# Kernel optimization log

Hardware: AMD Instinct MI355X
Metric: run time of the kernel (lower is better)

## Reference

```python
import jax, jax.numpy as jnp
import numpy as np

N_NODES = 50000
N_EDGES = 800000
N_GRAPHS = 64
IN_DIM = 128
HID = 256
N_LAYERS = 4
N_PROT = 5
N_CLASSES = 1
EPS = 1e-12


def setup_inputs() -> dict:
    key = jax.random.key(0)
    ks = jax.random.split(key, 10)
    h = jax.random.normal(ks[0], (N_NODES, IN_DIM), jnp.float32)
    src = jax.random.randint(ks[1], (N_EDGES,), 0, N_NODES, dtype=jnp.int32)
    dst = jax.random.randint(ks[2], (N_EDGES,), 0, N_NODES, dtype=jnp.int32)
    graph_id = jnp.sort(jax.random.randint(ks[3], (N_NODES,), 0, N_GRAPHS, dtype=jnp.int32))
    W_emb = jax.random.normal(ks[4], (IN_DIM, HID), jnp.float32) * 0.05
    b_emb = jnp.zeros((HID,), jnp.float32)
    Ws = jax.random.normal(ks[5], (N_LAYERS, 2 * HID, HID), jnp.float32) * 0.05
    bs = jnp.zeros((N_LAYERS, HID), jnp.float32)
    p_pos = jax.random.uniform(ks[6], (N_PROT, HID), jnp.float32)
    p_neg = jax.random.uniform(ks[7], (N_PROT, HID), jnp.float32)
    W_fc = jax.random.normal(ks[8], (N_CLASSES, 2 * N_PROT), jnp.float32) * 0.1
    return dict(h=h, src=src, dst=dst, graph_id=graph_id, W_emb=W_emb,
                b_emb=b_emb, Ws=Ws, bs=bs, p_pos=p_pos, p_neg=p_neg, W_fc=W_fc)


def _segment_mean(x, seg, num):
    # sum over segments, divide by count (empty segments -> 0, like DGL mean)
    s = jax.ops.segment_sum(x, seg, num_segments=num)
    cnt = jax.ops.segment_sum(jnp.ones((x.shape[0],), x.dtype), seg, num_segments=num)
    return s / jnp.maximum(cnt, 1.0)[:, None]


def _forward(h, src, dst, graph_id, W_emb, b_emb, Ws, bs, p_pos, p_neg, W_fc):
    x = h @ W_emb + b_emb  # [N, HID]
    for l in range(N_LAYERS):
        # mean aggregation of neighbor messages (copy_src -> mean at dst)
        c = _segment_mean(x[src], dst, N_NODES)  # [N, HID]
        bundle = jnp.concatenate([x, c], axis=1) @ Ws[l] + bs[l]  # [N, HID]
        # F.normalize(p=2, dim=1) then relu activation, then residual add
        norm = jnp.linalg.norm(bundle, axis=1, keepdims=True)
        bundle = bundle / jnp.maximum(norm, EPS)
        x = x + jax.nn.relu(bundle)
    hg = _segment_mean(x, graph_id, N_GRAPHS)  # dgl.mean_nodes -> [G, HID]

    def sims(P):
        d = jnp.sum((hg[:, None, :] - P[None, :, :]) ** 2, axis=-1)  # [G, P]
        return jnp.log((d + 1.0) / (d + EPS))

    ss = jnp.concatenate([sims(p_pos), sims(p_neg)], axis=1)  # [G, 2P]
    y = ss @ W_fc.T  # [G, n_classes]
    return jax.nn.sigmoid(y).squeeze()


def reference(h, src, dst, graph_id, W_emb, b_emb, Ws, bs, p_pos, p_neg, W_fc):
    return _forward(h, src, dst, graph_id, W_emb, b_emb, Ws, bs, p_pos, p_neg, W_fc)
```

## Files before the change

kernel.cpp:

```cpp
#include <hip/hip_runtime.h>
#include <math.h>

#define N_NODESC 50000
#define NPAD 50048
#define N_EDGESC 800000
#define N_GRAPHSC 64
#define IN_DIMC 128
#define HIDC 256
#define N_LAYERSC 4
#define EPSV 1e-12f

#define NBUCK 196
#define EPB 4096
#define NBLK1 196

typedef __attribute__((ext_vector_type(8))) short short8;
typedef __attribute__((ext_vector_type(4))) float floatx4;
typedef __attribute__((ext_vector_type(2))) float floatx2;

__device__ __forceinline__ unsigned short f2b(float f) {
    union { float f; unsigned u; } v; v.f = f;
    unsigned r = v.u + 0x7FFFu + ((v.u >> 16) & 1u);
    return (unsigned short)(r >> 16);
}
__device__ __forceinline__ float blo(unsigned u) { return __uint_as_float(u << 16); }
__device__ __forceinline__ float bhi(unsigned u) { return __uint_as_float(u & 0xFFFF0000u); }
__device__ __forceinline__ unsigned pkb(float a, float b) {
    return (unsigned)f2b(a) | ((unsigned)f2b(b) << 16);
}
__device__ __forceinline__ float b2f(unsigned short s) {
    return __uint_as_float((unsigned)s << 16);
}
__device__ __forceinline__ unsigned char f2q(float v) {
    return (unsigned char)(__builtin_amdgcn_cvt_pk_fp8_f32(v, v, 0, false) & 0xFF);
}
__device__ __forceinline__ float q2f(unsigned u) {
    floatx2 t = __builtin_amdgcn_cvt_pk_f32_fp8(u, false);
    return t.x;
}
__device__ __forceinline__ unsigned pk4q(float a, float b, float c, float d) {
    unsigned lo = (unsigned)__builtin_amdgcn_cvt_pk_fp8_f32(a, b, 0, false) & 0xFFFFu;
    unsigned hi = (unsigned)__builtin_amdgcn_cvt_pk_fp8_f32(c, d, 0, false) << 16;
    return lo | hi;
}
__device__ __forceinline__ void ldscp16(const void* g, void* l) {
    __builtin_amdgcn_global_load_lds(
        (const __attribute__((address_space(1))) unsigned int*)g,
        (__attribute__((address_space(3))) unsigned int*)l, 16, 0, 0);
}

__global__ __launch_bounds__(128) void k_gbounds(const int* __restrict__ gid,
        int* __restrict__ gstart) {
    int g = threadIdx.x;
    if (g > N_GRAPHSC) return;
    int lo = 0, hi = N_NODESC;
    while (lo < hi) {
        int mid = (lo + hi) >> 1;
        if (gid[mid] < g) lo = mid + 1; else hi = mid;
    }
    gstart[g] = lo;
}

__global__ __launch_bounds__(256) void k_bcount(const int* __restrict__ dst,
        int* __restrict__ gbcnt) {
    __shared__ int bc[256];
    int t = threadIdx.x;
    bc[t] = 0;
    __syncthreads();
    int e0 = blockIdx.x * EPB;
    for (int i = t; i < EPB; i += 256) {
        int e = e0 + i;
        if (e < N_EDGESC) atomicAdd(&bc[dst[e] >> 8], 1);
    }
    __syncthreads();
    if (t < NBUCK && bc[t] > 0) atomicAdd(&gbcnt[t], bc[t]);
}

__global__ __launch_bounds__(256) void k_bscan(const int* __restrict__ gbcnt,
        int* __restrict__ boffB, int* __restrict__ gcurB) {
    __shared__ int s[256];
    int t = threadIdx.x;
    int v = (t < NBUCK) ? gbcnt[t] : 0;
    s[t] = v;
    __syncthreads();
    for (int d = 1; d < 256; d <<= 1) {
        int u = (t >= d) ? s[t - d] : 0;
        __syncthreads();
        s[t] += u;
        __syncthreads();
    }
    if (t < NBUCK) {
        int excl = s[t] - v;
        boffB[t] = excl;
        gcurB[t] = excl;
    }
    if (t == 0) boffB[NBUCK] = N_EDGESC;
}

__global__ __launch_bounds__(256) void k_bscatter(const int* __restrict__ src,
        const int* __restrict__ dst, int* __restrict__ gcurB,
        unsigned* __restrict__ ebpack) {
    __shared__ int bc[256];
    __shared__ int cur[256];
    int t = threadIdx.x;
    bc[t] = 0;
    __syncthreads();
    int e0 = blockIdx.x * EPB;
    for (int i = t; i < EPB; i += 256) {
        int e = e0 + i;
        if (e < N_EDGESC) atomicAdd(&bc[dst[e] >> 8], 1);
    }
    __syncthreads();
    if (t < NBUCK)
        cur[t] = (bc[t] > 0) ? atomicAdd(&gcurB[t], bc[t]) : 0;
    __syncthreads();
    for (int i = t; i < EPB; i += 256) {
        int e = e0 + i;
        if (e < N_EDGESC) {
            int d = dst[e];
            int b = d >> 8;
            int pos = atomicAdd(&cur[b], 1);
            ebpack[pos] = (unsigned)src[e] | ((unsigned)(d & 255) << 16);
        }
    }
}

__global__ __launch_bounds__(256) void k_bbuild(const unsigned* __restrict__ ebpack,
        const int* __restrict__ boffB, int* __restrict__ offs,
        unsigned short* __restrict__ esrc) {
    __shared__ int deg[256];
    __shared__ int lofs[256];
    __shared__ unsigned short img[12288];
    int b = blockIdx.x;
    int t = threadIdx.x;
    int bbase = boffB[b];
    int cnt = boffB[b + 1] - bbase;
    deg[t] = 0;
    __syncthreads();
    for (int i = t; i < cnt; i += 256)
        atomicAdd(&deg[ebpack[bbase + i] >> 16], 1);
    __syncthreads();
    int v = deg[t];
    lofs[t] = v;
    __syncthreads();
    for (int d = 1; d < 256; d <<= 1) {
        int u = (t >= d) ? lofs[t - d] : 0;
        __syncthreads();
        lofs[t] += u;
        __syncthreads();
    }
    int excl = lofs[t] - v;
    int node = b * 256 + t;
    if (node < N_NODESC) offs[node] = bbase + excl;
    if (b == NBUCK - 1 && t == 0) offs[N_NODESC] = N_EDGESC;
    deg[t] = excl;
    __syncthreads();
    for (int i = t; i < cnt; i += 256) {
        unsigned p = ebpack[bbase + i];
        int pos = atomicAdd(&deg[p >> 16], 1);
        img[pos] = (unsigned short)(p & 0xFFFF);
    }
    __syncthreads();
    for (int i = t; i < cnt; i += 256)
        esrc[bbase + i] = img[i];
}

__global__ __launch_bounds__(256) void k_wconv(const float* __restrict__ Wemb,
        const float* __restrict__ Ws, unsigned short* __restrict__ wsw,
        unsigned char* __restrict__ wq) {
    int idx = blockIdx.x * 256 + threadIdx.x;
    const int EMB = IN_DIMC * HIDC;
    const int LYR = 2 * HIDC * HIDC;
    if (idx >= EMB + N_LAYERSC * LYR) return;
    if (idx < EMB) {
        int k = idx >> 8, n = idx & 255;
        int off = (((k >> 5) * 16 + (n >> 4)) * 64 + ((((k >> 3) & 3) << 4) | (n & 15))) * 8 + (k & 7);
        wsw[off] = f2b(Wemb[idx]);
    } else {
        int r = idx - EMB;
        int l = r >> 17;
        int r2 = r & (LYR - 1);
        int k = r2 >> 8, n = r2 & 255;
        int off = (((k >> 5) * 16 + (n >> 4)) * 64 + ((((k >> 3) & 3) << 4) | (n & 15))) * 8 + (k & 7);
        wq[(size_t)l * LYR + off] = f2q(Ws[r]);
    }
}

__global__ __launch_bounds__(256) void k_aggregate(const unsigned char* __restrict__ xq,
        const int* __restrict__ offs, const unsigned short* __restrict__ esrc,
        unsigned char* __restrict__ cq) {
    int gidx = blockIdx.x * 256 + threadIdx.x;
    int node = gidx >> 5;
    int lane = threadIdx.x & 31;
    if (node >= N_NODESC) return;
    int beg = offs[node], end = offs[node + 1];
    float a[8];
    #pragma unroll
    for (int j = 0; j < 8; j++) a[j] = 0.f;
    size_t loff = (size_t)lane * 8;
    int e = beg;
    #define ACC8(v) do { \
        floatx2 t0 = __builtin_amdgcn_cvt_pk_f32_fp8((v).x, false); \
        floatx2 t1 = __builtin_amdgcn_cvt_pk_f32_fp8((v).x, true);  \
        floatx2 t2 = __builtin_amdgcn_cvt_pk_f32_fp8((v).y, false); \
        floatx2 t3 = __builtin_amdgcn_cvt_pk_f32_fp8((v).y, true);  \
        a[0] += t0.x; a[1] += t0.y; a[2] += t1.x; a[3] += t1.y;     \
        a[4] += t2.x; a[5] += t2.y; a[6] += t3.x; a[7] += t3.y;     \
    } while (0)
    for (; e + 8 <= end; e += 8) {
        int sidx[8];
        #pragma unroll
        for (int j = 0; j < 8; j++) sidx[j] = esrc[e + j];
        uint2 v[8];
        #pragma unroll
        for (int j = 0; j < 8; j++)
            v[j] = *(const uint2*)(xq + (size_t)sidx[j] * HIDC + loff);
        #pragma unroll
        for (int j = 0; j < 8; j++) ACC8(v[j]);
    }
    if (e + 4 <= end) {
        int sidx[4];
        #pragma unroll
        for (int j = 0; j < 4; j++) sidx[j] = esrc[e + j];
        uint2 v[4];
        #pragma unroll
        for (int j = 0; j < 4; j++)
            v[j] = *(const uint2*)(xq + (size_t)sidx[j] * HIDC + loff);
        #pragma unroll
        for (int j = 0; j < 4; j++) ACC8(v[j]);
        e += 4;
    }
    for (; e < end; e++) {
        uint2 v = *(const uint2*)(xq + (size_t)esrc[e] * HIDC + loff);
        ACC8(v);
    }
    #undef ACC8
    float w = 1.0f / (float)max(end - beg, 1);
    uint2 o;
    o.x = pk4q(a[0] * w, a[1] * w, a[2] * w, a[3] * w);
    o.y = pk4q(a[4] * w, a[5] * w, a[6] * w, a[7] * w);
    *(uint2*)(cq + (size_t)node * HIDC + loff) = o;
}

template<bool LAST>
__global__ __launch_bounds__(256, 6) void k_lgemm(unsigned short* __restrict__ xb,
        unsigned char* __restrict__ xq, const unsigned char* __restrict__ cq,
        const unsigned char* __restrict__ wq, const float* __restrict__ bias) {
    __shared__ unsigned long long panelA64[1024];
    __shared__ unsigned long long panelC64[1024];
    __shared__ float rs[32];
    unsigned char* panelA = (unsigned char*)panelA64;
    unsigned char* panelC = (unsigned char*)panelC64;
    int tid = threadIdx.x;
    int w = tid >> 6;
    int lane = tid & 63;
    int quad = lane >> 4;
    int l15 = lane & 15;
    int row0 = blockIdx.x * 32;

    {
        int sboff = w * 2048 + lane * 16;
        #pragma unroll
        for (int i = 0; i < 2; i++) {
            int ldsoff = sboff + i * 1024;
            int r = ldsoff >> 8;
            int ch = (ldsoff & 255) >> 4;
            int lc = ch ^ (r & 15);
            ldscp16(xq + (size_t)(row0 + r) * HIDC + lc * 16, &panelA[w * 2048 + i * 1024]);
            ldscp16(cq + (size_t)(row0 + r) * HIDC + lc * 16, &panelC[w * 2048 + i * 1024]);
        }
    }
    __syncthreads();

    floatx4 acc[2][4];
    #pragma unroll
    for (int mt = 0; mt < 2; mt++)
        #pragma unroll
        for (int n = 0; n < 4; n++)
            acc[mt][n] = (floatx4){0.f, 0.f, 0.f, 0.f};

    const unsigned char* bp = wq + ((size_t)(w * 4) * 64 + lane) * 8;

    #pragma unroll
    for (int st = 0; st < 16; st++) {
        const unsigned char* pan = (st < 8) ? panelA : panelC;
        int ks = st & 7;
        long long afr[2], bfr[4];
        #pragma unroll
        for (int mt = 0; mt < 2; mt++) {
            int row = mt * 16 + l15;
            int lc = ks * 2 + (quad >> 1);
            int phys = lc ^ (row & 15);
            afr[mt] = *(const long long*)&pan[row * 256 + phys * 16 + (quad & 1) * 8];
        }
        const unsigned char* wp = bp + (size_t)st * 8192;
        #pragma unroll
        for (int n = 0; n < 4; n++)
            bfr[n] = *(const long long*)(wp + n * 512);
        #pragma unroll
        for (int mt = 0; mt < 2; mt++)
            #pragma unroll
            for (int n = 0; n < 4; n++)
                acc[mt][n] = __builtin_amdgcn_mfma_f32_16x16x32_fp8_fp8(
                    afr[mt], bfr[n], acc[mt][n], 0, 0, 0);
    }

    float bv[4];
    #pragma unroll
    for (int n = 0; n < 4; n++) bv[n] = bias[w * 64 + n * 16 + l15];
    #pragma unroll
    for (int mt = 0; mt < 2; mt++)
        #pragma unroll
        for (int n = 0; n < 4; n++)
            #pragma unroll
            for (int r = 0; r < 4; r++)
                acc[mt][n][r] += bv[n];

    __syncthreads();
    if (tid < 32) rs[tid] = 0.f;
    __syncthreads();
    #pragma unroll
    for (int mt = 0; mt < 2; mt++) {
        #pragma unroll
        for (int r = 0; r < 4; r++) {
            float p = acc[mt][0][r] * acc[mt][0][r] + acc[mt][1][r] * acc[mt][1][r]
                    + acc[mt][2][r] * acc[mt][2][r] + acc[mt][3][r] * acc[mt][3][r];
            p += __shfl_xor(p, 1);
            p += __shfl_xor(p, 2);
            p += __shfl_xor(p, 4);
            p += __shfl_xor(p, 8);
            if (l15 == 0) atomicAdd(&rs[mt * 16 + quad * 4 + r], p);
        }
    }
    __syncthreads();

    #pragma unroll
    for (int mt = 0; mt < 2; mt++) {
        #pragma unroll
        for (int r = 0; r < 4; r++) {
            int lrow = mt * 16 + quad * 4 + r;
            int row = row0 + lrow;
            if (row < N_NODESC) {
                float inv = 1.0f / fmaxf(sqrtf(rs[mt * 16 + quad * 4 + r]), EPSV);
                #pragma unroll
                for (int n = 0; n < 4; n++) {
                    int col = w * 64 + n * 16 + l15;
                    int phys = (w * 4 + n) ^ (lrow & 15);
                    float xo = q2f((unsigned)panelA[lrow * 256 + phys * 16 + l15]);
                    float v = fmaxf(acc[mt][n][r] * inv, 0.f);
                    float nv = xo + v;
                    size_t idx = (size_t)row * HIDC + col;
                    if (LAST) xb[idx] = f2b(nv);
                    else      xq[idx] = f2q(nv);
                }
            }
        }
    }
}

__global__ __launch_bounds__(256, 4) void k_egemm(const float* __restrict__ h,
        const unsigned short* __restrict__ wsw, const float* __restrict__ bias,
        unsigned char* __restrict__ xq) {
    int tid = threadIdx.x;
    int wn = tid >> 6;
    int lane = tid & 63;
    int quad = lane >> 4;
    int l15 = lane & 15;
    int row0 = blockIdx.x * 32;

    floatx4 acc[2][4];
    #pragma unroll
    for (int mt = 0; mt < 2; mt++)
        #pragma unroll
        for (int n = 0; n < 4; n++)
            acc[mt][n] = (floatx4){0.f, 0.f, 0.f, 0.f};

    int r0 = row0 + l15;
    int r1 = row0 + 16 + l15;
    bool ok0 = r0 < N_NODESC, ok1 = r1 < N_NODESC;
    const float* h0 = h + (size_t)r0 * IN_DIMC + quad * 8;
    const float* h1 = h + (size_t)r1 * IN_DIMC + quad * 8;
    const unsigned short* bp = wsw + ((size_t)(wn * 4) * 64 + lane) * 8;

    #pragma unroll
    for (int ks = 0; ks < 4; ks++) {
        float4 f00 = ok0 ? *(const float4*)(h0 + ks * 32)     : (float4){0,0,0,0};
        float4 f01 = ok0 ? *(const float4*)(h0 + ks * 32 + 4) : (float4){0,0,0,0};
        float4 f10 = ok1 ? *(const float4*)(h1 + ks * 32)     : (float4){0,0,0,0};
        float4 f11 = ok1 ? *(const float4*)(h1 + ks * 32 + 4) : (float4){0,0,0,0};
        short8 afr[2], bfr[4];
        uint4 av;
        av.x = pkb(f00.x, f00.y); av.y = pkb(f00.z, f00.w);
        av.z = pkb(f01.x, f01.y); av.w = pkb(f01.z, f01.w);
        afr[0] = *(short8*)&av;
        av.x = pkb(f10.x, f10.y); av.y = pkb(f10.z, f10.w);
        av.z = pkb(f11.x, f11.y); av.w = pkb(f11.z, f11.w);
        afr[1] = *(short8*)&av;
        const unsigned short* wp = bp + (size_t)ks * 8192;
        #pragma unroll
        for (int n = 0; n < 4; n++)
            bfr[n] = *(const short8*)(wp + n * 512);
        #pragma unroll
        for (int mt = 0; mt < 2; mt++)
            #pragma unroll
            for (int n = 0; n < 4; n++)
                acc[mt][n] = __builtin_amdgcn_mfma_f32_16x16x32_bf16(
                    afr[mt], bfr[n], acc[mt][n], 0, 0, 0);
    }

    float bv[4];
    #pragma unroll
    for (int n = 0; n < 4; n++) bv[n] = bias[wn * 64 + n * 16 + l15];
    #pragma unroll
    for (int mt = 0; mt < 2; mt++) {
        #pragma unroll
        for (int r = 0; r < 4; r++) {
            int row = row0 + mt * 16 + quad * 4 + r;
            if (row < N_NODESC) {
                #pragma unroll
                for (int n = 0; n < 4; n++) {
                    int col = wn * 64 + n * 16 + l15;
                    float v = acc[mt][n][r] + bv[n];
                    xq[(size_t)row * HIDC + col] = f2q(v);
                }
            }
        }
    }
}

__global__ __launch_bounds__(256) void k_pool(const unsigned short* __restrict__ xb,
        const int* __restrict__ gstart, float* __restrict__ hg) {
    __shared__ float red[256][8];
    int g = blockIdx.x >> 2;
    int cq = blockIdx.x & 3;
    int t = threadIdx.x;
    int cchunk = t & 7;
    int rgrp = t >> 3;
    int col0 = cq * 64 + cchunk * 8;
    int beg = gstart[g], end = gstart[g + 1];
    float a[8];
    #pragma unroll
    for (int j = 0; j < 8; j++) a[j] = 0.f;
    for (int r = beg + rgrp; r < end; r += 32) {
        uint4 v = *(const uint4*)(xb + (size_t)r * HIDC + col0);
        a[0] += blo(v.x); a[1] += bhi(v.x);
        a[2] += blo(v.y); a[3] += bhi(v.y);
        a[4] += blo(v.z); a[5] += bhi(v.z);
        a[6] += blo(v.w); a[7] += bhi(v.w);
    }
    #pragma unroll
    for (int j = 0; j < 8; j++) red[t][j] = a[j];
    __syncthreads();
    for (int d = 16; d >= 1; d >>= 1) {
        if (rgrp < d) {
            #pragma unroll
            for (int j = 0; j < 8; j++) red[t][j] += red[t + d * 8][j];
        }
        __syncthreads();
    }
    if (rgrp == 0) {
        float inv = 1.0f / (float)max(end - beg, 1);
        #pragma unroll
        for (int j = 0; j < 8; j++)
            hg[g * HIDC + col0 + j] = red[t][j] * inv;
    }
}

__global__ __launch_bounds__(256) void k_readout(const float* __restrict__ hg,
        const float* __restrict__ ppos, const float* __restrict__ pneg,
        const float* __restrict__ wfc, float* __restrict__ out) {
    __shared__ float red[256];
    __shared__ float ss[10];
    int t = threadIdx.x;
    int g = blockIdx.x;
    float hgv = hg[g * HIDC + t];
    for (int p = 0; p < 10; p++) {
        const float* P = (p < 5) ? (ppos + p * HIDC) : (pneg + (p - 5) * HIDC);
        float d = hgv - P[t];
        red[t] = d * d;
        __syncthreads();
        for (int s2 = 128; s2 > 0; s2 >>= 1) {
            if (t < s2) red[t] += red[t + s2];
            __syncthreads();
        }
        if (t == 0) {
            float dd = red[0];
            ss[p] = logf((dd + 1.0f) / (dd + EPSV));
        }
        __syncthreads();
    }
    if (t == 0) {
        float y = 0.f;
        #pragma unroll
        for (int p = 0; p < 10; p++) y += ss[p] * wfc[p];
        out[g] = 1.0f / (1.0f + expf(-y));
    }
}

extern "C" void kernel_launch(void* const* d_in, const int* in_sizes, int n_in,
                              void* d_out, int out_size, void* d_ws, size_t ws_size,
                              hipStream_t stream) {
    const float* h    = (const float*)d_in[0];
    const int*   src  = (const int*)d_in[1];
    const int*   dst  = (const int*)d_in[2];
    const int*   gid  = (const int*)d_in[3];
    const float* Wemb = (const float*)d_in[4];
    const float* bemb = (const float*)d_in[5];
    const float* Ws   = (const float*)d_in[6];
    const float* bs   = (const float*)d_in[7];
    const float* ppos = (const float*)d_in[8];
    const float* pneg = (const float*)d_in[9];
    const float* wfc  = (const float*)d_in[10];
    float* out = (float*)d_out;

    char* ws = (char*)d_ws;
    size_t off = 0;
    auto alloc = [&](size_t bytes) {
        void* p = ws + off;
        off += (bytes + 255) & ~(size_t)255;
        return p;
    };
    unsigned short* xb     = (unsigned short*)alloc((size_t)NPAD * HIDC * 2);
    unsigned char*  xq     = (unsigned char*)alloc((size_t)NPAD * HIDC);
    unsigned char*  cq     = (unsigned char*)alloc((size_t)NPAD * HIDC);
    unsigned short* wsw    = (unsigned short*)alloc((size_t)(IN_DIMC * HIDC) * 2);
    unsigned char*  wq     = (unsigned char*)alloc((size_t)(N_LAYERSC * 2 * HIDC * HIDC));
    int*            offs   = (int*)alloc((size_t)(N_NODESC + 1) * 4);
    unsigned short* esrc   = (unsigned short*)alloc((size_t)N_EDGESC * 2);
    unsigned*       ebpack = (unsigned*)alloc((size_t)N_EDGESC * 4);
    int*            gbcnt  = (int*)alloc((size_t)NBUCK * 4);
    int*            boffB  = (int*)alloc((size_t)(NBUCK + 1) * 4);
    int*            gcurB  = (int*)alloc((size_t)NBUCK * 4);
    int*            gstart = (int*)alloc((size_t)(N_GRAPHSC + 1) * 4);
    float*          hg     = (float*)alloc((size_t)N_GRAPHSC * HIDC * 4);
    (void)ws_size; (void)in_sizes; (void)n_in; (void)out_size;

    hipMemsetAsync(gbcnt, 0, (size_t)NBUCK * 4, stream);

    const int WTOT = IN_DIMC * HIDC + N_LAYERSC * 2 * HIDC * HIDC;
    k_wconv<<<(WTOT + 255) / 256, 256, 0, stream>>>(Wemb, Ws, wsw, wq);
    k_gbounds<<<1, 128, 0, stream>>>(gid, gstart);
    k_bcount<<<NBLK1, 256, 0, stream>>>(dst, gbcnt);
    k_bscan<<<1, 256, 0, stream>>>(gbcnt, boffB, gcurB);
    k_bscatter<<<NBLK1, 256, 0, stream>>>(src, dst, gcurB, ebpack);
    k_bbuild<<<NBUCK, 256, 0, stream>>>(ebpack, boffB, offs, esrc);

    k_egemm<<<NPAD / 32, 256, 0, stream>>>(h, wsw, bemb, xq);

    for (int l = 0; l < N_LAYERSC; l++) {
        k_aggregate<<<(N_NODESC * 32 + 255) / 256, 256, 0, stream>>>(xq, offs, esrc, cq);
        if (l < N_LAYERSC - 1)
            k_lgemm<false><<<NPAD / 32, 256, 0, stream>>>(
                xb, xq, cq, wq + (size_t)l * 2 * HIDC * HIDC, bs + (size_t)l * HIDC);
        else
            k_lgemm<true><<<NPAD / 32, 256, 0, stream>>>(
                xb, xq, cq, wq + (size_t)l * 2 * HIDC * HIDC, bs + (size_t)l * HIDC);
    }
    k_pool<<<N_GRAPHSC * 4, 256, 0, stream>>>(xb, gstart, hg);
    k_readout<<<N_GRAPHSC, 256, 0, stream>>>(hg, ppos, pneg, wfc, out);
}
```

Measured before the change: 397.0 us.

## Fuse aggregation into layer GEMM, fuse pooling, merge preprocessing kernels

```diff
diff --git a/kernel.cpp b/kernel.cpp
--- a/kernel.cpp
+++ b/kernel.cpp
@@ -13,6 +13,7 @@
 #define NBUCK 196
 #define EPB 4096
 #define NBLK1 196
+#define WCONV_BLKS 2176
 
 typedef __attribute__((ext_vector_type(8))) short short8;
 typedef __attribute__((ext_vector_type(4))) float floatx4;
@@ -23,13 +24,8 @@
     unsigned r = v.u + 0x7FFFu + ((v.u >> 16) & 1u);
     return (unsigned short)(r >> 16);
 }
-__device__ __forceinline__ float blo(unsigned u) { return __uint_as_float(u << 16); }
-__device__ __forceinline__ float bhi(unsigned u) { return __uint_as_float(u & 0xFFFF0000u); }
 __device__ __forceinline__ unsigned pkb(float a, float b) {
     return (unsigned)f2b(a) | ((unsigned)f2b(b) << 16);
-}
-__device__ __forceinline__ float b2f(unsigned short s) {
-    return __uint_as_float((unsigned)s << 16);
 }
 __device__ __forceinline__ unsigned char f2q(float v) {
     return (unsigned char)(__builtin_amdgcn_cvt_pk_fp8_f32(v, v, 0, false) & 0xFF);
@@ -48,32 +44,60 @@
         (const __attribute__((address_space(1))) unsigned int*)g,
         (__attribute__((address_space(3))) unsigned int*)l, 16, 0, 0);
 }
-
-__global__ __launch_bounds__(128) void k_gbounds(const int* __restrict__ gid,
-        int* __restrict__ gstart) {
-    int g = threadIdx.x;
-    if (g > N_GRAPHSC) return;
-    int lo = 0, hi = N_NODESC;
-    while (lo < hi) {
-        int mid = (lo + hi) >> 1;
-        if (gid[mid] < g) lo = mid + 1; else hi = mid;
-    }
-    gstart[g] = lo;
-}
-
-__global__ __launch_bounds__(256) void k_bcount(const int* __restrict__ dst,
+__device__ __forceinline__ void acc8(uint2 v, float* a) {
+    floatx2 t0 = __builtin_amdgcn_cvt_pk_f32_fp8(v.x, false);
+    floatx2 t1 = __builtin_amdgcn_cvt_pk_f32_fp8(v.x, true);
+    floatx2 t2 = __builtin_amdgcn_cvt_pk_f32_fp8(v.y, false);
+    floatx2 t3 = __builtin_amdgcn_cvt_pk_f32_fp8(v.y, true);
+    a[0] += t0.x; a[1] += t0.y; a[2] += t1.x; a[3] += t1.y;
+    a[4] += t2.x; a[5] += t2.y; a[6] += t3.x; a[7] += t3.y;
+}
+
+__global__ __launch_bounds__(256) void k_pre1(const float* __restrict__ Wemb,
+        const float* __restrict__ Ws, unsigned short* __restrict__ wsw,
+        unsigned char* __restrict__ wq, const int* __restrict__ gid,
+        int* __restrict__ gstart, const int* __restrict__ dst,
         int* __restrict__ gbcnt) {
     __shared__ int bc[256];
+    int b = blockIdx.x;
     int t = threadIdx.x;
-    bc[t] = 0;
-    __syncthreads();
-    int e0 = blockIdx.x * EPB;
-    for (int i = t; i < EPB; i += 256) {
-        int e = e0 + i;
-        if (e < N_EDGESC) atomicAdd(&bc[dst[e] >> 8], 1);
-    }
-    __syncthreads();
-    if (t < NBUCK && bc[t] > 0) atomicAdd(&gbcnt[t], bc[t]);
+    if (b < WCONV_BLKS) {
+        int idx = b * 256 + t;
+        const int EMB = IN_DIMC * HIDC;
+        const int LYR = 2 * HIDC * HIDC;
+        if (idx < EMB) {
+            int k = idx >> 8, n = idx & 255;
+            int off = (((k >> 5) * 16 + (n >> 4)) * 64 + ((((k >> 3) & 3) << 4) | (n & 15))) * 8 + (k & 7);
+            wsw[off] = f2b(Wemb[idx]);
+        } else if (idx < EMB + N_LAYERSC * LYR) {
+            int r = idx - EMB;
+            int l = r >> 17;
+            int r2 = r & (LYR - 1);
+            int k = r2 >> 8, n = r2 & 255;
+            int off = (((k >> 5) * 16 + (n >> 4)) * 64 + ((((k >> 3) & 3) << 4) | (n & 15))) * 8 + (k & 7);
+            wq[(size_t)l * LYR + off] = f2q(Ws[r]);
+        }
+    } else if (b == WCONV_BLKS) {
+        int g = t;
+        if (g <= N_GRAPHSC) {
+            int lo = 0, hi = N_NODESC;
+            while (lo < hi) {
+                int mid = (lo + hi) >> 1;
+                if (gid[mid] < g) lo = mid + 1; else hi = mid;
+            }
+            gstart[g] = lo;
+        }
+    } else {
+        bc[t] = 0;
+        __syncthreads();
+        int e0 = (b - WCONV_BLKS - 1) * EPB;
+        for (int i = t; i < EPB; i += 256) {
+            int e = e0 + i;
+            if (e < N_EDGESC) atomicAdd(&bc[dst[e] >> 8], 1);
+        }
+        __syncthreads();
+        if (t < NBUCK && bc[t] > 0) atomicAdd(&gbcnt[t], bc[t]);
+    }
 }
 
 __global__ __launch_bounds__(256) void k_bscan(const int* __restrict__ gbcnt,
@@ -97,276 +121,43 @@
     if (t == 0) boffB[NBUCK] = N_EDGESC;
 }
 
-__global__ __launch_bounds__(256) void k_bscatter(const int* __restrict__ src,
+__global__ __launch_bounds__(256, 4) void k_scat_egemm(const int* __restrict__ src,
         const int* __restrict__ dst, int* __restrict__ gcurB,
-        unsigned* __restrict__ ebpack) {
+        unsigned* __restrict__ ebpack, const float* __restrict__ h,
+        const unsigned short* __restrict__ wsw, const float* __restrict__ bias,
+        unsigned char* __restrict__ xq) {
     __shared__ int bc[256];
     __shared__ int cur[256];
-    int t = threadIdx.x;
-    bc[t] = 0;
-    __syncthreads();
-    int e0 = blockIdx.x * EPB;
-    for (int i = t; i < EPB; i += 256) {
-        int e = e0 + i;
-        if (e < N_EDGESC) atomicAdd(&bc[dst[e] >> 8], 1);
-    }
-    __syncthreads();
-    if (t < NBUCK)
-        cur[t] = (bc[t] > 0) ? atomicAdd(&gcurB[t], bc[t]) : 0;
-    __syncthreads();
-    for (int i = t; i < EPB; i += 256) {
-        int e = e0 + i;
-        if (e < N_EDGESC) {
-            int d = dst[e];
-            int b = d >> 8;
-            int pos = atomicAdd(&cur[b], 1);
-            ebpack[pos] = (unsigned)src[e] | ((unsigned)(d & 255) << 16);
-        }
-    }
-}
-
-__global__ __launch_bounds__(256) void k_bbuild(const unsigned* __restrict__ ebpack,
-        const int* __restrict__ boffB, int* __restrict__ offs,
-        unsigned short* __restrict__ esrc) {
-    __shared__ int deg[256];
-    __shared__ int lofs[256];
-    __shared__ unsigned short img[12288];
-    int b = blockIdx.x;
-    int t = threadIdx.x;
-    int bbase = boffB[b];
-    int cnt = boffB[b + 1] - bbase;
-    deg[t] = 0;
-    __syncthreads();
-    for (int i = t; i < cnt; i += 256)
-        atomicAdd(&deg[ebpack[bbase + i] >> 16], 1);
-    __syncthreads();
-    int v = deg[t];
-    lofs[t] = v;
-    __syncthreads();
-    for (int d = 1; d < 256; d <<= 1) {
-        int u = (t >= d) ? lofs[t - d] : 0;
-        __syncthreads();
-        lofs[t] += u;
-        __syncthreads();
-    }
-    int excl = lofs[t] - v;
-    int node = b * 256 + t;
-    if (node < N_NODESC) offs[node] = bbase + excl;
-    if (b == NBUCK - 1 && t == 0) offs[N_NODESC] = N_EDGESC;
-    deg[t] = excl;
-    __syncthreads();
-    for (int i = t; i < cnt; i += 256) {
-        unsigned p = ebpack[bbase + i];
-        int pos = atomicAdd(&deg[p >> 16], 1);
-        img[pos] = (unsigned short)(p & 0xFFFF);
-    }
-    __syncthreads();
-    for (int i = t; i < cnt; i += 256)
-        esrc[bbase + i] = img[i];
-}
-
-__global__ __launch_bounds__(256) void k_wconv(const float* __restrict__ Wemb,
-        const float* __restrict__ Ws, unsigned short* __restrict__ wsw,
-        unsigned char* __restrict__ wq) {
-    int idx = blockIdx.x * 256 + threadIdx.x;
-    const int EMB = IN_DIMC * HIDC;
-    const int LYR = 2 * HIDC * HIDC;
-    if (idx >= EMB + N_LAYERSC * LYR) return;
-    if (idx < EMB) {
-        int k = idx >> 8, n = idx & 255;
-        int off = (((k >> 5) * 16 + (n >> 4)) * 64 + ((((k >> 3) & 3) << 4) | (n & 15))) * 8 + (k & 7);
-        wsw[off] = f2b(Wemb[idx]);
-    } else {
-        int r = idx - EMB;
-        int l = r >> 17;
-        int r2 = r & (LYR - 1);
-        int k = r2 >> 8, n = r2 & 255;
-        int off = (((k >> 5) * 16 + (n >> 4)) * 64 + ((((k >> 3) & 3) << 4) | (n & 15))) * 8 + (k & 7);
-        wq[(size_t)l * LYR + off] = f2q(Ws[r]);
-    }
-}
-
-__global__ __launch_bounds__(256) void k_aggregate(const unsigned char* __restrict__ xq,
-        const int* __restrict__ offs, const unsigned short* __restrict__ esrc,
-        unsigned char* __restrict__ cq) {
-    int gidx = blockIdx.x * 256 + threadIdx.x;
-    int node = gidx >> 5;
-    int lane = threadIdx.x & 31;
-    if (node >= N_NODESC) return;
-    int beg = offs[node], end = offs[node + 1];
-    float a[8];
-    #pragma unroll
-    for (int j = 0; j < 8; j++) a[j] = 0.f;
-    size_t loff = (size_t)lane * 8;
-    int e = beg;
-    #define ACC8(v) do { \
-        floatx2 t0 = __builtin_amdgcn_cvt_pk_f32_fp8((v).x, false); \
-        floatx2 t1 = __builtin_amdgcn_cvt_pk_f32_fp8((v).x, true);  \
-        floatx2 t2 = __builtin_amdgcn_cvt_pk_f32_fp8((v).y, false); \
-        floatx2 t3 = __builtin_amdgcn_cvt_pk_f32_fp8((v).y, true);  \
-        a[0] += t0.x; a[1] += t0.y; a[2] += t1.x; a[3] += t1.y;     \
-        a[4] += t2.x; a[5] += t2.y; a[6] += t3.x; a[7] += t3.y;     \
-    } while (0)
-    for (; e + 8 <= end; e += 8) {
-        int sidx[8];
-        #pragma unroll
-        for (int j = 0; j < 8; j++) sidx[j] = esrc[e + j];
-        uint2 v[8];
-        #pragma unroll
-        for (int j = 0; j < 8; j++)
-            v[j] = *(const uint2*)(xq + (size_t)sidx[j] * HIDC + loff);
-        #pragma unroll
-        for (int j = 0; j < 8; j++) ACC8(v[j]);
-    }
-    if (e + 4 <= end) {
-        int sidx[4];
-        #pragma unroll
-        for (int j = 0; j < 4; j++) sidx[j] = esrc[e + j];
-        uint2 v[4];
-        #pragma unroll
-        for (int j = 0; j < 4; j++)
-            v[j] = *(const uint2*)(xq + (size_t)sidx[j] * HIDC + loff);
-        #pragma unroll
-        for (int j = 0; j < 4; j++) ACC8(v[j]);
-        e += 4;
-    }
-    for (; e < end; e++) {
-        uint2 v = *(const uint2*)(xq + (size_t)esrc[e] * HIDC + loff);
-        ACC8(v);
-    }
-    #undef ACC8
-    float w = 1.0f / (float)max(end - beg, 1);
-    uint2 o;
-    o.x = pk4q(a[0] * w, a[1] * w, a[2] * w, a[3] * w);
-    o.y = pk4q(a[4] * w, a[5] * w, a[6] * w, a[7] * w);
-    *(uint2*)(cq + (size_t)node * HIDC + loff) = o;
-}
-
-template<bool LAST>
-__global__ __launch_bounds__(256, 6) void k_lgemm(unsigned short* __restrict__ xb,
-        unsigned char* __restrict__ xq, const unsigned char* __restrict__ cq,
-        const unsigned char* __restrict__ wq, const float* __restrict__ bias) {
-    __shared__ unsigned long long panelA64[1024];
-    __shared__ unsigned long long panelC64[1024];
-    __shared__ float rs[32];
-    unsigned char* panelA = (unsigned char*)panelA64;
-    unsigned char* panelC = (unsigned char*)panelC64;
-    int tid = threadIdx.x;
-    int w = tid >> 6;
-    int lane = tid & 63;
-    int quad = lane >> 4;
-    int l15 = lane & 15;
-    int row0 = blockIdx.x * 32;
-
-    {
-        int sboff = w * 2048 + lane * 16;
-        #pragma unroll
-        for (int i = 0; i < 2; i++) {
-            int ldsoff = sboff + i * 1024;
-            int r = ldsoff >> 8;
-            int ch = (ldsoff & 255) >> 4;
-            int lc = ch ^ (r & 15);
-            ldscp16(xq + (size_t)(row0 + r) * HIDC + lc * 16, &panelA[w * 2048 + i * 1024]);
-            ldscp16(cq + (size_t)(row0 + r) * HIDC + lc * 16, &panelC[w * 2048 + i * 1024]);
-        }
-    }
-    __syncthreads();
-
-    floatx4 acc[2][4];
-    #pragma unroll
-    for (int mt = 0; mt < 2; mt++)
-        #pragma unroll
-        for (int n = 0; n < 4; n++)
-            acc[mt][n] = (floatx4){0.f, 0.f, 0.f, 0.f};
-
-    const unsigned char* bp = wq + ((size_t)(w * 4) * 64 + lane) * 8;
-
-    #pragma unroll
-    for (int st = 0; st < 16; st++) {
-        const unsigned char* pan = (st < 8) ? panelA : panelC;
-        int ks = st & 7;
-        long long afr[2], bfr[4];
-        #pragma unroll
-        for (int mt = 0; mt < 2; mt++) {
-            int row = mt * 16 + l15;
-            int lc = ks * 2 + (quad >> 1);
-            int phys = lc ^ (row & 15);
-            afr[mt] = *(const long long*)&pan[row * 256 + phys * 16 + (quad & 1) * 8];
-        }
-        const unsigned char* wp = bp + (size_t)st * 8192;
-        #pragma unroll
-        for (int n = 0; n < 4; n++)
-            bfr[n] = *(const long long*)(wp + n * 512);
-        #pragma unroll
-        for (int mt = 0; mt < 2; mt++)
-            #pragma unroll
-            for (int n = 0; n < 4; n++)
-                acc[mt][n] = __builtin_amdgcn_mfma_f32_16x16x32_fp8_fp8(
-                    afr[mt], bfr[n], acc[mt][n], 0, 0, 0);
-    }
-
-    float bv[4];
-    #pragma unroll
-    for (int n = 0; n < 4; n++) bv[n] = bias[w * 64 + n * 16 + l15];
-    #pragma unroll
-    for (int mt = 0; mt < 2; mt++)
-        #pragma unroll
-        for (int n = 0; n < 4; n++)
-            #pragma unroll
-            for (int r = 0; r < 4; r++)
-                acc[mt][n][r] += bv[n];
-
-    __syncthreads();
-    if (tid < 32) rs[tid] = 0.f;
-    __syncthreads();
-    #pragma unroll
-    for (int mt = 0; mt < 2; mt++) {
-        #pragma unroll
-        for (int r = 0; r < 4; r++) {
-            float p = acc[mt][0][r] * acc[mt][0][r] + acc[mt][1][r] * acc[mt][1][r]
-                    + acc[mt][2][r] * acc[mt][2][r] + acc[mt][3][r] * acc[mt][3][r];
-            p += __shfl_xor(p, 1);
-            p += __shfl_xor(p, 2);
-            p += __shfl_xor(p, 4);
-            p += __shfl_xor(p, 8);
-            if (l15 == 0) atomicAdd(&rs[mt * 16 + quad * 4 + r], p);
-        }
-    }
-    __syncthreads();
-
-    #pragma unroll
-    for (int mt = 0; mt < 2; mt++) {
-        #pragma unroll
-        for (int r = 0; r < 4; r++) {
-            int lrow = mt * 16 + quad * 4 + r;
-            int row = row0 + lrow;
-            if (row < N_NODESC) {
-                float inv = 1.0f / fmaxf(sqrtf(rs[mt * 16 + quad * 4 + r]), EPSV);
-                #pragma unroll
-                for (int n = 0; n < 4; n++) {
-                    int col = w * 64 + n * 16 + l15;
-                    int phys = (w * 4 + n) ^ (lrow & 15);
-                    float xo = q2f((unsigned)panelA[lrow * 256 + phys * 16 + l15]);
-                    float v = fmaxf(acc[mt][n][r] * inv, 0.f);
-                    float nv = xo + v;
-                    size_t idx = (size_t)row * HIDC + col;
-                    if (LAST) xb[idx] = f2b(nv);
-                    else      xq[idx] = f2q(nv);
-                }
-            }
-        }
-    }
-}
-
-__global__ __launch_bounds__(256, 4) void k_egemm(const float* __restrict__ h,
-        const unsigned short* __restrict__ wsw, const float* __restrict__ bias,
-        unsigned char* __restrict__ xq) {
+    if (blockIdx.x < NBLK1) {
+        int t = threadIdx.x;
+        bc[t] = 0;
+        __syncthreads();
+        int e0 = blockIdx.x * EPB;
+        for (int i = t; i < EPB; i += 256) {
+            int e = e0 + i;
+            if (e < N_EDGESC) atomicAdd(&bc[dst[e] >> 8], 1);
+        }
+        __syncthreads();
+        if (t < NBUCK)
+            cur[t] = (bc[t] > 0) ? atomicAdd(&gcurB[t], bc[t]) : 0;
+        __syncthreads();
+        for (int i = t; i < EPB; i += 256) {
+            int e = e0 + i;
+            if (e < N_EDGESC) {
+                int d = dst[e];
+                int b = d >> 8;
+                int pos = atomicAdd(&cur[b], 1);
+                ebpack[pos] = (unsigned)src[e] | ((unsigned)(d & 255) << 16);
+            }
+        }
+        return;
+    }
     int tid = threadIdx.x;
     int wn = tid >> 6;
     int lane = tid & 63;
     int quad = lane >> 4;
     int l15 = lane & 15;
-    int row0 = blockIdx.x * 32;
+    int row0 = (blockIdx.x - NBLK1) * 32;
 
     floatx4 acc[2][4];
     #pragma unroll
@@ -428,52 +219,247 @@
     }
 }
 
-__global__ __launch_bounds__(256) void k_pool(const unsigned short* __restrict__ xb,
-        const int* __restrict__ gstart, float* __restrict__ hg) {
-    __shared__ float red[256][8];
-    int g = blockIdx.x >> 2;
-    int cq = blockIdx.x & 3;
+__global__ __launch_bounds__(256) void k_bbuild(const unsigned* __restrict__ ebpack,
+        const int* __restrict__ boffB, int* __restrict__ offs,
+        unsigned short* __restrict__ esrc) {
+    __shared__ int deg[256];
+    __shared__ int lofs[256];
+    __shared__ unsigned short img[12288];
+    int b = blockIdx.x;
     int t = threadIdx.x;
-    int cchunk = t & 7;
-    int rgrp = t >> 3;
-    int col0 = cq * 64 + cchunk * 8;
-    int beg = gstart[g], end = gstart[g + 1];
-    float a[8];
-    #pragma unroll
-    for (int j = 0; j < 8; j++) a[j] = 0.f;
-    for (int r = beg + rgrp; r < end; r += 32) {
-        uint4 v = *(const uint4*)(xb + (size_t)r * HIDC + col0);
-        a[0] += blo(v.x); a[1] += bhi(v.x);
-        a[2] += blo(v.y); a[3] += bhi(v.y);
-        a[4] += blo(v.z); a[5] += bhi(v.z);
-        a[6] += blo(v.w); a[7] += bhi(v.w);
-    }
-    #pragma unroll
-    for (int j = 0; j < 8; j++) red[t][j] = a[j];
-    __syncthreads();
-    for (int d = 16; d >= 1; d >>= 1) {
-        if (rgrp < d) {
+    int bbase = boffB[b];
+    int cnt = boffB[b + 1] - bbase;
+    deg[t] = 0;
+    __syncthreads();
+    for (int i = t; i < cnt; i += 256)
+        atomicAdd(&deg[ebpack[bbase + i] >> 16], 1);
+    __syncthreads();
+    int v = deg[t];
+    lofs[t] = v;
+    __syncthreads();
+    for (int d = 1; d < 256; d <<= 1) {
+        int u = (t >= d) ? lofs[t - d] : 0;
+        __syncthreads();
+        lofs[t] += u;
+        __syncthreads();
+    }
+    int excl = lofs[t] - v;
+    int node = b * 256 + t;
+    if (node < N_NODESC) offs[node] = bbase + excl;
+    if (b == NBUCK - 1 && t == 0) offs[N_NODESC] = N_EDGESC;
+    deg[t] = excl;
+    __syncthreads();
+    for (int i = t; i < cnt; i += 256) {
+        unsigned p = ebpack[bbase + i];
+        int pos = atomicAdd(&deg[p >> 16], 1);
+        img[pos] = (unsigned short)(p & 0xFFFF);
+    }
+    __syncthreads();
+    for (int i = t; i < cnt; i += 256)
+        esrc[bbase + i] = img[i];
+}
+
+template<bool LAST>
+__global__ __launch_bounds__(256, 6) void k_layer(const unsigned char* __restrict__ xqin,
+        unsigned char* __restrict__ xqout, const unsigned char* __restrict__ wq,
+        const float* __restrict__ bias, const int* __restrict__ offs,
+        const unsigned short* __restrict__ esrc, const int* __restrict__ gid,
+        float* __restrict__ hg) {
+    __shared__ unsigned long long panelA64[1024];
+    __shared__ unsigned long long panelC64[1024];
+    __shared__ float rs[32];
+    __shared__ float hgp[LAST ? 1024 : 1];
+    __shared__ signed char ggl[LAST ? 32 : 1];
+    __shared__ int g0s;
+    unsigned char* panelA = (unsigned char*)panelA64;
+    unsigned char* panelC = (unsigned char*)panelC64;
+    int tid = threadIdx.x;
+    int w = tid >> 6;
+    int lane = tid & 63;
+    int quad = lane >> 4;
+    int l15 = lane & 15;
+    int row0 = blockIdx.x * 32;
+
+    {
+        int sboff = w * 2048 + lane * 16;
+        #pragma unroll
+        for (int i = 0; i < 2; i++) {
+            int ldsoff = sboff + i * 1024;
+            int r = ldsoff >> 8;
+            int ch = (ldsoff & 255) >> 4;
+            int lc = ch ^ (r & 15);
+            ldscp16(xqin + (size_t)(row0 + r) * HIDC + lc * 16, &panelA[w * 2048 + i * 1024]);
+        }
+    }
+
+    {
+        int lane32 = tid & 31;
+        int sub = tid >> 5;
+        size_t loff = (size_t)lane32 * 8;
+        #pragma unroll 1
+        for (int grp = 0; grp < 4; grp++) {
+            int lrow = grp * 8 + sub;
+            int node = row0 + lrow;
+            float a[8];
             #pragma unroll
-            for (int j = 0; j < 8; j++) red[t][j] += red[t + d * 8][j];
-        }
-        __syncthreads();
-    }
-    if (rgrp == 0) {
-        float inv = 1.0f / (float)max(end - beg, 1);
-        #pragma unroll
-        for (int j = 0; j < 8; j++)
-            hg[g * HIDC + col0 + j] = red[t][j] * inv;
+            for (int j = 0; j < 8; j++) a[j] = 0.f;
+            int beg = 0, end = 0;
+            if (node < N_NODESC) { beg = offs[node]; end = offs[node + 1]; }
+            int e = beg;
+            for (; e + 8 <= end; e += 8) {
+                int sidx[8];
+                #pragma unroll
+                for (int j = 0; j < 8; j++) sidx[j] = esrc[e + j];
+                uint2 v[8];
+                #pragma unroll
+                for (int j = 0; j < 8; j++)
+                    v[j] = *(const uint2*)(xqin + (size_t)sidx[j] * HIDC + loff);
+                #pragma unroll
+                for (int j = 0; j < 8; j++) acc8(v[j], a);
+            }
+            if (e + 4 <= end) {
+                int sidx[4];
+                #pragma unroll
+                for (int j = 0; j < 4; j++) sidx[j] = esrc[e + j];
+                uint2 v[4];
+                #pragma unroll
+                for (int j = 0; j < 4; j++)
+                    v[j] = *(const uint2*)(xqin + (size_t)sidx[j] * HIDC + loff);
+                #pragma unroll
+                for (int j = 0; j < 4; j++) acc8(v[j], a);
+                e += 4;
+            }
+            for (; e < end; e++) {
+                uint2 v = *(const uint2*)(xqin + (size_t)esrc[e] * HIDC + loff);
+                acc8(v, a);
+            }
+            float wm = 1.0f / (float)max(end - beg, 1);
+            uint2 o;
+            o.x = pk4q(a[0] * wm, a[1] * wm, a[2] * wm, a[3] * wm);
+            o.y = pk4q(a[4] * wm, a[5] * wm, a[6] * wm, a[7] * wm);
+            int phys = (lane32 >> 1) ^ (lrow & 15);
+            *(uint2*)&panelC[lrow * 256 + phys * 16 + (lane32 & 1) * 8] = o;
+        }
+    }
+    __syncthreads();
+
+    floatx4 acc[2][4];
+    #pragma unroll
+    for (int mt = 0; mt < 2; mt++)
+        #pragma unroll
+        for (int n = 0; n < 4; n++)
+            acc[mt][n] = (floatx4){0.f, 0.f, 0.f, 0.f};
+
+    const unsigned char* bp = wq + ((size_t)(w * 4) * 64 + lane) * 8;
+
+    #pragma unroll
+    for (int st = 0; st < 16; st++) {
+        const unsigned char* pan = (st < 8) ? panelA : panelC;
+        int ks = st & 7;
+        long long afr[2], bfr[4];
+        #pragma unroll
+        for (int mt = 0; mt < 2; mt++) {
+            int row = mt * 16 + l15;
+            int lc = ks * 2 + (quad >> 1);
+            int phys = lc ^ (row & 15);
+            afr[mt] = *(const long long*)&pan[row * 256 + phys * 16 + (quad & 1) * 8];
+        }
+        const unsigned char* wp = bp + (size_t)st * 8192;
+        #pragma unroll
+        for (int n = 0; n < 4; n++)
+            bfr[n] = *(const long long*)(wp + n * 512);
+        #pragma unroll
+        for (int mt = 0; mt < 2; mt++)
+            #pragma unroll
+            for (int n = 0; n < 4; n++)
+                acc[mt][n] = __builtin_amdgcn_mfma_f32_16x16x32_fp8_fp8(
+                    afr[mt], bfr[n], acc[mt][n], 0, 0, 0);
+    }
+
+    float bv[4];
+    #pragma unroll
+    for (int n = 0; n < 4; n++) bv[n] = bias[w * 64 + n * 16 + l15];
+    #pragma unroll
+    for (int mt = 0; mt < 2; mt++)
+        #pragma unroll
+        for (int n = 0; n < 4; n++)
+            #pragma unroll
+            for (int r = 0; r < 4; r++)
+                acc[mt][n][r] += bv[n];
+
+    __syncthreads();
+    if (tid < 32) rs[tid] = 0.f;
+    if constexpr (LAST) {
+        #pragma unroll
+        for (int i = 0; i < 4; i++) hgp[i * 256 + tid] = 0.f;
+        if (tid < 32) {
+            int g0 = gid[min(row0, N_NODESC - 1)];
+            int gv = gid[min(row0 + tid, N_NODESC - 1)] - g0;
+            ggl[tid] = (signed char)min(gv, 3);
+            if (tid == 0) g0s = g0;
+        }
+    }
+    __syncthreads();
+    #pragma unroll
+    for (int mt = 0; mt < 2; mt++) {
+        #pragma unroll
+        for (int r = 0; r < 4; r++) {
+            float p = acc[mt][0][r] * acc[mt][0][r] + acc[mt][1][r] * acc[mt][1][r]
+                    + acc[mt][2][r] * acc[mt][2][r] + acc[mt][3][r] * acc[mt][3][r];
+            p += __shfl_xor(p, 1);
+            p += __shfl_xor(p, 2);
+            p += __shfl_xor(p, 4);
+            p += __shfl_xor(p, 8);
+            if (l15 == 0) atomicAdd(&rs[mt * 16 + quad * 4 + r], p);
+        }
+    }
+    __syncthreads();
+
+    #pragma unroll
+    for (int mt = 0; mt < 2; mt++) {
+        #pragma unroll
+        for (int r = 0; r < 4; r++) {
+            int lrow = mt * 16 + quad * 4 + r;
+            int row = row0 + lrow;
+            if (row < N_NODESC) {
+                float inv = 1.0f / fmaxf(sqrtf(rs[mt * 16 + quad * 4 + r]), EPSV);
+                #pragma unroll
+                for (int n = 0; n < 4; n++) {
+                    int col = w * 64 + n * 16 + l15;
+                    int phys = (w * 4 + n) ^ (lrow & 15);
+                    float xo = q2f((unsigned)panelA[lrow * 256 + phys * 16 + l15]);
+                    float nv = xo + fmaxf(acc[mt][n][r] * inv, 0.f);
+                    if constexpr (LAST) {
+                        atomicAdd(&hgp[(int)ggl[lrow] * 256 + col], nv);
+                    } else {
+                        xqout[(size_t)row * HIDC + col] = f2q(nv);
+                    }
+                }
+            }
+        }
+    }
+    if constexpr (LAST) {
+        __syncthreads();
+        if (row0 < N_NODESC) {
+            int nspan = (int)ggl[31] + 1;
+            int g0 = g0s;
+            for (int gl = 0; gl < nspan; gl++)
+                atomicAdd(&hg[(g0 + gl) * HIDC + tid], hgp[gl * 256 + tid]);
+        }
     }
 }
 
 __global__ __launch_bounds__(256) void k_readout(const float* __restrict__ hg,
-        const float* __restrict__ ppos, const float* __restrict__ pneg,
-        const float* __restrict__ wfc, float* __restrict__ out) {
+        const int* __restrict__ gstart, const float* __restrict__ ppos,
+        const float* __restrict__ pneg, const float* __restrict__ wfc,
+        float* __restrict__ out) {
     __shared__ float red[256];
     __shared__ float ss[10];
     int t = threadIdx.x;
     int g = blockIdx.x;
-    float hgv = hg[g * HIDC + t];
+    int beg = gstart[g], end = gstart[g + 1];
+    float inv = 1.0f / (float)max(end - beg, 1);
+    float hgv = hg[g * HIDC + t] * inv;
     for (int p = 0; p < 10; p++) {
         const float* P = (p < 5) ? (ppos + p * HIDC) : (pneg + (p - 5) * HIDC);
         float d = hgv - P[t];
@@ -520,9 +506,8 @@
         off += (bytes + 255) & ~(size_t)255;
         return p;
     };
-    unsigned short* xb     = (unsigned short*)alloc((size_t)NPAD * HIDC * 2);
-    unsigned char*  xq     = (unsigned char*)alloc((size_t)NPAD * HIDC);
-    unsigned char*  cq     = (unsigned char*)alloc((size_t)NPAD * HIDC);
+    unsigned char*  xqA    = (unsigned char*)alloc((size_t)NPAD * HIDC);
+    unsigned char*  xqB    = (unsigned char*)alloc((size_t)NPAD * HIDC);
     unsigned short* wsw    = (unsigned short*)alloc((size_t)(IN_DIMC * HIDC) * 2);
     unsigned char*  wq     = (unsigned char*)alloc((size_t)(N_LAYERSC * 2 * HIDC * HIDC));
     int*            offs   = (int*)alloc((size_t)(N_NODESC + 1) * 4);
@@ -536,26 +521,18 @@
     (void)ws_size; (void)in_sizes; (void)n_in; (void)out_size;
 
     hipMemsetAsync(gbcnt, 0, (size_t)NBUCK * 4, stream);
-
-    const int WTOT = IN_DIMC * HIDC + N_LAYERSC * 2 * HIDC * HIDC;
-    k_wconv<<<(WTOT + 255) / 256, 256, 0, stream>>>(Wemb, Ws, wsw, wq);
-    k_gbounds<<<1, 128, 0, stream>>>(gid, gstart);
-    k_bcount<<<NBLK1, 256, 0, stream>>>(dst, gbcnt);
+    hipMemsetAsync(hg, 0, (size_t)N_GRAPHSC * HIDC * 4, stream);
+
+    const int LYR = 2 * HIDC * HIDC;
+    k_pre1<<<WCONV_BLKS + 1 + NBLK1, 256, 0, stream>>>(Wemb, Ws, wsw, wq, gid, gstart, dst, gbcnt);
     k_bscan<<<1, 256, 0, stream>>>(gbcnt, boffB, gcurB);
-    k_bscatter<<<NBLK1, 256, 0, stream>>>(src, dst, gcurB, ebpack);
+    k_scat_egemm<<<NBLK1 + NPAD / 32, 256, 0, stream>>>(src, dst, gcurB, ebpack, h, wsw, bemb, xqA);
     k_bbuild<<<NBUCK, 256, 0, stream>>>(ebpack, boffB, offs, esrc);
 
-    k_egemm<<<NPAD / 32, 256, 0, stream>>>(h, wsw, bemb, xq);
-
-    for (int l = 0; l < N_LAYERSC; l++) {
-        k_aggregate<<<(N_NODESC * 32 + 255) / 256, 256, 0, stream>>>(xq, offs, esrc, cq);
-        if (l < N_LAYERSC - 1)
-            k_lgemm<false><<<NPAD / 32, 256, 0, stream>>>(
-                xb, xq, cq, wq + (size_t)l * 2 * HIDC * HIDC, bs + (size_t)l * HIDC);
-        else
-            k_lgemm<true><<<NPAD / 32, 256, 0, stream>>>(
-                xb, xq, cq, wq + (size_t)l * 2 * HIDC * HIDC, bs + (size_t)l * HIDC);
-    }
-    k_pool<<<N_GRAPHSC * 4, 256, 0, stream>>>(xb, gstart, hg);
-    k_readout<<<N_GRAPHSC, 256, 0, stream>>>(hg, ppos, pneg, wfc, out);
-}
+    k_layer<false><<<NPAD / 32, 256, 0, stream>>>(xqA, xqB, wq + (size_t)0 * LYR, bs + 0 * HIDC, offs, esrc, gid, hg);
+    k_layer<false><<<NPAD / 32, 256, 0, stream>>>(xqB, xqA, wq + (size_t)1 * LYR, bs + 1 * HIDC, offs, esrc, gid, hg);
+    k_layer<false><<<NPAD / 32, 256, 0, stream>>>(xqA, xqB, wq + (size_t)2 * LYR, bs + 2 * HIDC, offs, esrc, gid, hg);
+    k_layer<true ><<<NPAD / 32, 256, 0, stream>>>(xqB, xqA, wq + (size_t)3 * LYR, bs + 3 * HIDC, offs, esrc, gid, hg);
+
+    k_readout<<<N_GRAPHSC, 256, 0, stream>>>(hg, gstart, ppos, pneg, wfc, out);
+}
```

After: 407.1 us. 2.5% more time.
